# Kernel tuning notes

Measured on AMD Instinct MI355X. Metric: run time of the kernel, lower is better.

## Reference

```python
import jax, jax.numpy as jnp
import numpy as np

B, N, F, R, H = 64, 128, 128, 64, 256
L = 3           # number of DTNN layers (hidden_dim=[256,256,256])
FC = 256        # fc_hidden_dim[0]
OUT = 1
SCALE = 0.05


def setup_inputs() -> dict:
    key = jax.random.key(0)
    ks = jax.random.split(key, 12)
    inp = {
        "x": jax.random.normal(ks[0], (B, N, F), dtype=jnp.float32),
        # RBF-expanded pairwise distances are nonnegative
        "distance": jax.random.uniform(ks[1], (B, N, N, R), dtype=jnp.float32),
        # stacked per-layer params (all layers share shapes since hidden dims equal)
        "Wcf_w": jax.random.normal(ks[2], (L, H, F), dtype=jnp.float32) * SCALE,
        "Wcf_b": jax.random.normal(ks[3], (L, H), dtype=jnp.float32) * SCALE,
        "Wdf_w": jax.random.normal(ks[4], (L, H, R), dtype=jnp.float32) * SCALE,
        "Wdf_b": jax.random.normal(ks[5], (L, H), dtype=jnp.float32) * SCALE,
        "Wfc_w": jax.random.normal(ks[6], (L, F, H), dtype=jnp.float32) * SCALE,  # no bias
        "fc0_w": jax.random.normal(ks[7], (FC, F), dtype=jnp.float32) * SCALE,
        "fc0_b": jax.random.normal(ks[8], (FC,), dtype=jnp.float32) * SCALE,
        "out_w": jax.random.normal(ks[9], (OUT, FC), dtype=jnp.float32) * SCALE,
        "out_b": jax.random.normal(ks[10], (OUT,), dtype=jnp.float32) * SCALE,
    }
    return inp


def reference(x, distance, Wcf_w, Wcf_b, Wdf_w, Wdf_b, Wfc_w, fc0_w, fc0_b, out_w, out_b):
    # Original per-layer math:
    #   msg_i = sum_j Wfc( Wcf(x_i) * Wdf(d_ij) )
    # Since Wcf(x_i) is independent of j and all maps are linear, this equals
    #   Wfc( Wcf(x_i) * (sum_j d_ij) @ Wdf_w^T + N * Wdf_b ),
    # which avoids materializing the (B,N,N,H) grid while computing identical math.
    n = x.shape[1]
    d_sum = jnp.sum(distance, axis=2)  # (B, N, R)
    for l in range(Wcf_w.shape[0]):
        cf = jnp.einsum('bnf,hf->bnh', x, Wcf_w[l]) + Wcf_b[l]            # (B,N,H)
        df = jnp.einsum('bnr,hr->bnh', d_sum, Wdf_w[l]) + n * Wdf_b[l]    # (B,N,H)
        h = jnp.einsum('bnh,fh->bnf', cf * df, Wfc_w[l])                  # (B,N,F)
        x = h + jnp.tanh(h)                                                # residual-tanh
    g = jnp.sum(x, axis=1)                     # sum pooling over nodes -> (B,F)
    g = g @ fc0_w.T + fc0_b                    # (B,FC)
    return g @ out_w.T + out_b                 # (B,OUT)
```

## Files before the change

kernel.cpp:

```cpp
#include <hip/hip_runtime.h>
#include <math.h>

#define B_ 64
#define N_ 128
#define F_ 128
#define R_ 64
#define H_ 256
#define L_ 3
#define M_ (B_*N_)

#define DS_PAD 72
#define X_PAD 136
#define P_PAD 264

#define PREPW_NBLK 48
#define COMB_BID   48
#define DSUM_BID0  49

typedef short bf16x8 __attribute__((ext_vector_type(8)));
typedef float f32x4 __attribute__((ext_vector_type(4)));

__device__ __forceinline__ unsigned short f2bf(float f) {
    unsigned int u = __float_as_uint(f);
    u += 0x7FFF + ((u >> 16) & 1);
    return (unsigned short)(u >> 16);
}

__device__ __forceinline__ float tanh_fast(float h) {
    float a = fabsf(h);
    float e = __expf(-2.0f * a);
    float t = (1.0f - e) * __builtin_amdgcn_rcpf(1.0f + e);
    return copysignf(t, h);
}

__global__ __launch_bounds__(256)
void dsum_prep_kernel(const float* __restrict__ dist,
                      const float* __restrict__ wcf,
                      const float* __restrict__ wdf,
                      const float* __restrict__ wfc,
                      const float* __restrict__ fc0_w, const float* __restrict__ fc0_b,
                      const float* __restrict__ out_w, const float* __restrict__ out_b,
                      unsigned short* __restrict__ wcfb,
                      unsigned short* __restrict__ wdfb,
                      unsigned short* __restrict__ wfcb,
                      float* __restrict__ wcomb,
                      unsigned short* __restrict__ dsumb,
                      float* __restrict__ out) {
    const int bid = blockIdx.x;
    const int t   = threadIdx.x;

    if (bid < PREPW_NBLK) {
        const int NCF = L_*H_*F_/4;
        const int NDF = L_*H_*R_/4;
        const int NFC = L_*F_*H_/4;
        const int total = NCF + NDF + NFC;
        for (int i = bid*256 + t; i < total; i += PREPW_NBLK*256) {
            const float4* src; unsigned short* dst; int k;
            if (i < NCF)           { src = (const float4*)wcf; dst = wcfb; k = i; }
            else if (i < NCF+NDF)  { src = (const float4*)wdf; dst = wdfb; k = i-NCF; }
            else                   { src = (const float4*)wfc; dst = wfcb; k = i-NCF-NDF; }
            float4 v = src[k];
            ushort4 o; o.x=f2bf(v.x); o.y=f2bf(v.y); o.z=f2bf(v.z); o.w=f2bf(v.w);
            ((ushort4*)dst)[k] = o;
        }
        return;
    }
    if (bid == COMB_BID) {
        if (t < 128) {
            float s = 0.f;
            #pragma unroll 8
            for (int c = 0; c < 256; ++c) s += out_w[c] * fc0_w[c*128 + t];
            wcomb[t] = s;
        } else if (t < 192) {
            float bb = out_b[0];
            #pragma unroll 8
            for (int c = 0; c < 256; ++c) bb += out_w[c] * fc0_b[c];
            out[t - 128] = bb;
        }
        return;
    }

    const int row = bid - DSUM_BID0;
    const float4* src = (const float4*)(dist + (size_t)row * (N_*R_));
    const int q = t & 15, jg = t >> 4;
    float4 a = make_float4(0.f,0.f,0.f,0.f);
    #pragma unroll
    for (int j0 = 0; j0 < N_; j0 += 16) {
        float4 v = src[(j0 + jg)*16 + q];
        a.x += v.x; a.y += v.y; a.z += v.z; a.w += v.w;
    }
    __shared__ float4 sh[256];
    sh[t] = a;
    __syncthreads();
    if (t < 16) {
        float4 s = sh[t];
        for (int g = 1; g < 16; ++g) {
            float4 v = sh[t + 16*g];
            s.x += v.x; s.y += v.y; s.z += v.z; s.w += v.w;
        }
        ushort4 o; o.x=f2bf(s.x); o.y=f2bf(s.y); o.z=f2bf(s.z); o.w=f2bf(s.w);
        ((ushort4*)(dsumb + (size_t)row * R_))[t] = o;
    }
}

__global__ __launch_bounds__(512)
void layers_kernel(const float* __restrict__ x,
                   const unsigned short* __restrict__ dsumb,
                   const unsigned short* __restrict__ wcfb,
                   const unsigned short* __restrict__ wdfb,
                   const unsigned short* __restrict__ wfcb,
                   const float* __restrict__ biascf,
                   const float* __restrict__ biasdf,
                   const float* __restrict__ wcomb,
                   float* __restrict__ out) {
    __shared__ __align__(16) unsigned short ds_lds[32][DS_PAD];
    __shared__ __align__(16) unsigned short x_lds[32][X_PAD];
    __shared__ __align__(16) unsigned short p_lds[32][P_PAD];

    const int g    = blockIdx.x;
    const int t    = threadIdx.x;
    const int w    = t >> 6, lane = t & 63;
    const int lr   = lane & 15, lg = lane >> 4;

    {
        const int row16 = t >> 4, q = t & 15;
        const float4* xs = (const float4*)(x + (size_t)(g*32 + row16)*F_ + q*8);
        float4 xv0 = xs[0], xv1 = xs[1];
        bf16x8 xb;
        xb[0]=f2bf(xv0.x); xb[1]=f2bf(xv0.y); xb[2]=f2bf(xv0.z); xb[3]=f2bf(xv0.w);
        xb[4]=f2bf(xv1.x); xb[5]=f2bf(xv1.y); xb[6]=f2bf(xv1.z); xb[7]=f2bf(xv1.w);
        *(bf16x8*)&x_lds[row16][q*8] = xb;
        if (t < 256) {
            const uint4* dsrc = (const uint4*)(dsumb + (size_t)(g*32 + (t>>3))*R_);
            uint4 v = dsrc[t & 7];
            *(uint4*)&ds_lds[t>>3][(t&7)*8] = v;
        }
    }
    __syncthreads();

    float pool_acc = 0.f;

    #pragma unroll 1
    for (int l = 0; l < L_; ++l) {
        const unsigned short* wcf = wcfb + l*H_*F_;
        const unsigned short* wdf = wdfb + l*H_*R_;
        const unsigned short* wfc = wfcb + l*F_*H_;

        bf16x8 xa[2][4], da[2][2];
        #pragma unroll
        for (int mh = 0; mh < 2; ++mh) {
            #pragma unroll
            for (int kc = 0; kc < 4; ++kc)
                xa[mh][kc] = *(const bf16x8*)&x_lds[mh*16 + lr][kc*32 + lg*8];
            #pragma unroll
            for (int kc = 0; kc < 2; ++kc)
                da[mh][kc] = *(const bf16x8*)&ds_lds[mh*16 + lr][kc*32 + lg*8];
        }

        #pragma unroll
        for (int nt = 0; nt < 2; ++nt) {
            const int ncol = w*32 + nt*16 + lr;
            bf16x8 bcfv[4], bdfv[2];
            #pragma unroll
            for (int kc = 0; kc < 4; ++kc)
                bcfv[kc] = *(const bf16x8*)(wcf + (size_t)ncol*F_ + kc*32 + lg*8);
            #pragma unroll
            for (int kc = 0; kc < 2; ++kc)
                bdfv[kc] = *(const bf16x8*)(wdf + (size_t)ncol*R_ + kc*32 + lg*8);
            const float bc = biascf[l*H_ + ncol];
            const float bd = biasdf[l*H_ + ncol] * 128.0f;
            #pragma unroll
            for (int mh = 0; mh < 2; ++mh) {
                f32x4 acf = {0.f,0.f,0.f,0.f}, adf = {0.f,0.f,0.f,0.f};
                #pragma unroll
                for (int kc = 0; kc < 4; ++kc)
                    acf = __builtin_amdgcn_mfma_f32_16x16x32_bf16(xa[mh][kc], bcfv[kc], acf, 0, 0, 0);
                #pragma unroll
                for (int kc = 0; kc < 2; ++kc)
                    adf = __builtin_amdgcn_mfma_f32_16x16x32_bf16(da[mh][kc], bdfv[kc], adf, 0, 0, 0);
                #pragma unroll
                for (int j = 0; j < 4; ++j) {
                    float p = (acf[j] + bc) * (adf[j] + bd);
                    p_lds[mh*16 + lg*4 + j][ncol] = f2bf(p);
                }
            }
        }
        __syncthreads();

        const int ncol2 = w*16 + lr;
        f32x4 ah[2] = {{0,0,0,0},{0,0,0,0}};
        #pragma unroll
        for (int kc = 0; kc < 8; ++kc) {
            bf16x8 b = *(const bf16x8*)(wfc + (size_t)ncol2*H_ + kc*32 + lg*8);
            #pragma unroll
            for (int mh = 0; mh < 2; ++mh) {
                bf16x8 ap = *(const bf16x8*)&p_lds[mh*16 + lr][kc*32 + lg*8];
                ah[mh] = __builtin_amdgcn_mfma_f32_16x16x32_bf16(ap, b, ah[mh], 0, 0, 0);
            }
        }
        __syncthreads();

        if (l < L_-1) {
            #pragma unroll
            for (int mh = 0; mh < 2; ++mh)
                #pragma unroll
                for (int j = 0; j < 4; ++j) {
                    float h = ah[mh][j];
                    float xo = h + tanh_fast(h);
                    x_lds[mh*16 + lg*4 + j][ncol2] = f2bf(xo);
                }
            __syncthreads();
        } else {
            const float wc = wcomb[ncol2];
            #pragma unroll
            for (int mh = 0; mh < 2; ++mh)
                #pragma unroll
                for (int j = 0; j < 4; ++j) {
                    float h = ah[mh][j];
                    pool_acc += (h + tanh_fast(h)) * wc;
                }
        }
    }

    float* red = (float*)&p_lds[0][0];
    red[t] = pool_acc;
    __syncthreads();
    #pragma unroll
    for (int s = 256; s > 0; s >>= 1) {
        if (t < s) red[t] += red[t + s];
        __syncthreads();
    }
    if (t == 0) atomicAdd(&out[g >> 2], red[0]);
}

extern "C" void kernel_launch(void* const* d_in, const int* in_sizes, int n_in,
                              void* d_out, int out_size, void* d_ws, size_t ws_size,
                              hipStream_t stream) {
    const float* x     = (const float*)d_in[0];
    const float* dist  = (const float*)d_in[1];
    const float* wcf_w = (const float*)d_in[2];
    const float* wcf_b = (const float*)d_in[3];
    const float* wdf_w = (const float*)d_in[4];
    const float* wdf_b = (const float*)d_in[5];
    const float* wfc_w = (const float*)d_in[6];
    const float* fc0_w = (const float*)d_in[7];
    const float* fc0_b = (const float*)d_in[8];
    const float* out_w = (const float*)d_in[9];
    const float* out_b = (const float*)d_in[10];
    float* out = (float*)d_out;

    char* ws = (char*)d_ws;
    unsigned short* wcfb  = (unsigned short*)(ws);
    unsigned short* wdfb  = (unsigned short*)(ws + 196608u);
    unsigned short* wfcb  = (unsigned short*)(ws + 294912u);
    float*          wcomb = (float*)(ws + 491520u);
    unsigned short* dsumb = (unsigned short*)(ws + 492032u);

    dsum_prep_kernel<<<DSUM_BID0 + M_, 256, 0, stream>>>(
        dist, wcf_w, wdf_w, wfc_w, fc0_w, fc0_b, out_w, out_b,
        wcfb, wdfb, wfcb, wcomb, dsumb, out);

    layers_kernel<<<M_/32, 512, 0, stream>>>(x, dsumb, wcfb, wdfb, wfcb,
                                             wcf_b, wdf_b, wcomb, out);
}
```

Baseline: 64.45 us.

## Double layers kernel block to 1024 threads and use shuffle reduction

Raises the layers kernel block from 8 to 16 wavefronts. Each wave now computes one 16-column tile in the first GEMM and one (row-half, column-group) tile in the Wfc GEMM, which halves per-wave MFMA work and register pressure. The final pooling reduction changes from a shared-memory tree with many barriers to wave shuffles plus a 16-entry shared array. The trade-off is that per-wave weight loads are no longer amortised across two M halves, and a larger block may limit occupancy and make barriers costlier.

After: 69.64 us. +8.1%, slower.

```diff
diff --git a/kernel.cpp b/kernel.cpp
--- a/kernel.cpp
+++ b/kernel.cpp
@@ -103,7 +103,7 @@
     }
 }
 
-__global__ __launch_bounds__(512)
+__global__ __launch_bounds__(1024)
 void layers_kernel(const float* __restrict__ x,
                    const unsigned short* __restrict__ dsumb,
                    const unsigned short* __restrict__ wcfb,
@@ -116,13 +116,15 @@
     __shared__ __align__(16) unsigned short ds_lds[32][DS_PAD];
     __shared__ __align__(16) unsigned short x_lds[32][X_PAD];
     __shared__ __align__(16) unsigned short p_lds[32][P_PAD];
+    __shared__ float wred[16];
 
     const int g    = blockIdx.x;
     const int t    = threadIdx.x;
     const int w    = t >> 6, lane = t & 63;
     const int lr   = lane & 15, lg = lane >> 4;
-
-    {
+    const int mh2  = w & 1,  ng = w >> 1;
+
+    if (t < 512) {
         const int row16 = t >> 4, q = t & 15;
         const float4* xs = (const float4*)(x + (size_t)(g*32 + row16)*F_ + q*8);
         float4 xv0 = xs[0], xv1 = xs[1];
@@ -130,11 +132,10 @@
         xb[0]=f2bf(xv0.x); xb[1]=f2bf(xv0.y); xb[2]=f2bf(xv0.z); xb[3]=f2bf(xv0.w);
         xb[4]=f2bf(xv1.x); xb[5]=f2bf(xv1.y); xb[6]=f2bf(xv1.z); xb[7]=f2bf(xv1.w);
         *(bf16x8*)&x_lds[row16][q*8] = xb;
-        if (t < 256) {
-            const uint4* dsrc = (const uint4*)(dsumb + (size_t)(g*32 + (t>>3))*R_);
-            uint4 v = dsrc[t & 7];
-            *(uint4*)&ds_lds[t>>3][(t&7)*8] = v;
-        }
+    } else if (t < 768) {
+        const int idx = t - 512, row = idx >> 3, c = idx & 7;
+        uint4 v = ((const uint4*)(dsumb + (size_t)(g*32 + row)*R_))[c];
+        *(uint4*)&ds_lds[row][c*8] = v;
     }
     __syncthreads();
 
@@ -157,9 +158,8 @@
                 da[mh][kc] = *(const bf16x8*)&ds_lds[mh*16 + lr][kc*32 + lg*8];
         }
 
-        #pragma unroll
-        for (int nt = 0; nt < 2; ++nt) {
-            const int ncol = w*32 + nt*16 + lr;
+        {
+            const int ncol = w*16 + lr;
             bf16x8 bcfv[4], bdfv[2];
             #pragma unroll
             for (int kc = 0; kc < 4; ++kc)
@@ -187,50 +187,45 @@
         }
         __syncthreads();
 
-        const int ncol2 = w*16 + lr;
-        f32x4 ah[2] = {{0,0,0,0},{0,0,0,0}};
+        const int ncol2 = ng*16 + lr;
+        f32x4 ah = {0.f,0.f,0.f,0.f};
         #pragma unroll
         for (int kc = 0; kc < 8; ++kc) {
-            bf16x8 b = *(const bf16x8*)(wfc + (size_t)ncol2*H_ + kc*32 + lg*8);
-            #pragma unroll
-            for (int mh = 0; mh < 2; ++mh) {
-                bf16x8 ap = *(const bf16x8*)&p_lds[mh*16 + lr][kc*32 + lg*8];
-                ah[mh] = __builtin_amdgcn_mfma_f32_16x16x32_bf16(ap, b, ah[mh], 0, 0, 0);
+            bf16x8 b  = *(const bf16x8*)(wfc + (size_t)ncol2*H_ + kc*32 + lg*8);
+            bf16x8 ap = *(const bf16x8*)&p_lds[mh2*16 + lr][kc*32 + lg*8];
+            ah = __builtin_amdgcn_mfma_f32_16x16x32_bf16(ap, b, ah, 0, 0, 0);
+        }
+        __syncthreads();
+
+        if (l < L_-1) {
+            #pragma unroll
+            for (int j = 0; j < 4; ++j) {
+                float h = ah[j];
+                float xo = h + tanh_fast(h);
+                x_lds[mh2*16 + lg*4 + j][ncol2] = f2bf(xo);
             }
-        }
-        __syncthreads();
-
-        if (l < L_-1) {
-            #pragma unroll
-            for (int mh = 0; mh < 2; ++mh)
-                #pragma unroll
-                for (int j = 0; j < 4; ++j) {
-                    float h = ah[mh][j];
-                    float xo = h + tanh_fast(h);
-                    x_lds[mh*16 + lg*4 + j][ncol2] = f2bf(xo);
-                }
             __syncthreads();
         } else {
             const float wc = wcomb[ncol2];
             #pragma unroll
-            for (int mh = 0; mh < 2; ++mh)
-                #pragma unroll
-                for (int j = 0; j < 4; ++j) {
-                    float h = ah[mh][j];
-                    pool_acc += (h + tanh_fast(h)) * wc;
-                }
-        }
-    }
-
-    float* red = (float*)&p_lds[0][0];
-    red[t] = pool_acc;
+            for (int j = 0; j < 4; ++j) {
+                float h = ah[j];
+                pool_acc += (h + tanh_fast(h)) * wc;
+            }
+        }
+    }
+
+    #pragma unroll
+    for (int off = 1; off < 64; off <<= 1)
+        pool_acc += __shfl_xor(pool_acc, off);
+    if (lane == 0) wred[w] = pool_acc;
     __syncthreads();
-    #pragma unroll
-    for (int s = 256; s > 0; s >>= 1) {
-        if (t < s) red[t] += red[t + s];
-        __syncthreads();
-    }
-    if (t == 0) atomicAdd(&out[g >> 2], red[0]);
+    if (t == 0) {
+        float s = 0.f;
+        #pragma unroll
+        for (int k = 0; k < 16; ++k) s += wred[k];
+        atomicAdd(&out[g >> 2], s);
+    }
 }
 
 extern "C" void kernel_launch(void* const* d_in, const int* in_sizes, int n_in,
@@ -260,6 +255,6 @@
         dist, wcf_w, wdf_w, wfc_w, fc0_w, fc0_b, out_w, out_b,
         wcfb, wdfb, wfcb, wcomb, dsumb, out);
 
-    layers_kernel<<<M_/32, 512, 0, stream>>>(x, dsumb, wcfb, wdfb, wfcb,
-                                             wcf_b, wdf_b, wcomb, out);
-}
+    layers_kernel<<<M_/32, 1024, 0, stream>>>(x, dsumb, wcfb, wdfb, wfcb,
+                                              wcf_b, wdf_b, wcomb, out);
+}
```
